# Kernel tuning notes

Measured on AMD Instinct MI355X. Metric: run time of the kernel, lower is better.

Reference implementation:

```python
import jax, jax.numpy as jnp
import numpy as np

LAMBDA_REG = 1.0  # default lambda_reg in MetaOptNetHead_Ridge_CS


def setup_inputs() -> dict:
    key = jax.random.key(0)
    k1, k2, k3 = jax.random.split(key, 3)
    B, n_query, n_support, d = 512, 75, 25, 1024
    n_way, n_shot = 5, 5
    query = jax.random.normal(k1, (B, n_query, d), dtype=jnp.float32)
    support = jax.random.normal(k2, (B, n_support, d), dtype=jnp.float32)
    support_labels = jax.random.randint(k3, (B, n_support), 0, n_way, dtype=jnp.int64)
    scale = jnp.ones((1,), dtype=jnp.float32)
    return {
        "query": query,
        "support": support,
        "support_labels": support_labels,
        "scale": scale,
        "n_way": n_way,
        "n_shot": n_shot,
    }


def reference(query, support, support_labels, scale, n_way, n_shot):
    # query:   (B, n_query, d)
    # support: (B, n_support, d), n_support == n_way * n_shot
    B, n_support, d = support.shape
    dtype = support.dtype
    # one-hot support labels: (B, n_support, n_way)
    Y = jax.nn.one_hot(support_labels, n_way, dtype=dtype)
    # K = S S^T + lambda I : (B, n_support, n_support)
    K = jnp.einsum("bnd,bmd->bnm", support, support) \
        + LAMBDA_REG * jnp.eye(n_support, dtype=dtype)
    # close_w = S^T K^{-1} Y  (computed via batched solve instead of explicit inverse)
    A = jnp.linalg.solve(K, Y)                    # (B, n_support, n_way)
    W = jnp.einsum("bnd,bnc->bdc", support, A)    # (B, d, n_way)
    logits = jnp.einsum("bqd,bdc->bqc", query, W)  # (B, n_query, n_way)
    return scale * logits
```

## Files before the change

kernel.cpp:

```cpp
#include <hip/hip_runtime.h>
#include <hip/hip_bf16.h>

#define NS 25
#define NW 5
#define D  1024
#define NQ 75
#define CHUNK 128
#define SPAD 132
#define NCHUNK (D / CHUNK)
#define WROW 1056

__global__ __launch_bounds__(256) void k_solve(const float* __restrict__ S,
                                               const int* __restrict__ labels,
                                               float* __restrict__ A_ws) {
    const int b = blockIdx.x;
    const int t = threadIdx.x;

    __shared__ float s_chunk[NS * SPAD];
    __shared__ float kpart[8 * NS * NS];
    __shared__ float M[NS * 33];
    __shared__ float prow[32];
    __shared__ float pcol[NS];

    const float* Sb = S + (size_t)b * NS * D;

    float acc[5][5];
    const int tile = t >> 3;
    const int sk   = t & 7;
    const int i0 = (tile / 5) * 5;
    const int j0 = (tile % 5) * 5;
    if (t < 200) {
#pragma unroll
        for (int a = 0; a < 5; ++a)
#pragma unroll
            for (int c = 0; c < 5; ++c) acc[a][c] = 0.f;
    }

    for (int ch = 0; ch < NCHUNK; ++ch) {
        for (int g = t; g < NS * 32; g += 256) {
            const int row = g >> 5;
            const int c4  = g & 31;
            float4 v = *reinterpret_cast<const float4*>(Sb + row * D + ch * CHUNK + c4 * 4);
            *reinterpret_cast<float4*>(&s_chunk[row * SPAD + c4 * 4]) = v;
        }
        __syncthreads();
        if (t < 200) {
#pragma unroll
            for (int ii = 0; ii < 4; ++ii) {
                const int kl = sk * 16 + ii * 4;
                float4 si[5], sj[5];
#pragma unroll
                for (int a = 0; a < 5; ++a)
                    si[a] = *reinterpret_cast<const float4*>(&s_chunk[(i0 + a) * SPAD + kl]);
#pragma unroll
                for (int a = 0; a < 5; ++a)
                    sj[a] = *reinterpret_cast<const float4*>(&s_chunk[(j0 + a) * SPAD + kl]);
#pragma unroll
                for (int a = 0; a < 5; ++a)
#pragma unroll
                    for (int c = 0; c < 5; ++c)
                        acc[a][c] += si[a].x * sj[c].x + si[a].y * sj[c].y +
                                     si[a].z * sj[c].z + si[a].w * sj[c].w;
            }
        }
        __syncthreads();
    }

    if (t < 200) {
#pragma unroll
        for (int a = 0; a < 5; ++a)
#pragma unroll
            for (int c = 0; c < 5; ++c)
                kpart[sk * NS * NS + (i0 + a) * NS + (j0 + c)] = acc[a][c];
    }
    __syncthreads();

    for (int item = t; item < NS * NS; item += 256) {
        const int i = item / NS, j = item % NS;
        float s = 0.f;
#pragma unroll
        for (int p = 0; p < 8; ++p) s += kpart[p * NS * NS + item];
        if (i == j) s += 1.0f;
        M[i * 33 + j] = s;
    }
    if (t < NS * NW) {
        const int i = t / NW, c = t % NW;
        const int lab = labels[b * NS + i];
        M[i * 33 + NS + c] = (lab == c) ? 1.f : 0.f;
    }
    __syncthreads();

    for (int p = 0; p < NS; ++p) {
        if (t < 30) prow[t] = M[p * 33 + t];
        if (t >= 32 && t < 32 + NS) pcol[t - 32] = M[(t - 32) * 33 + p];
        __syncthreads();
        const float finv = 1.0f / prow[p];
        for (int item = t; item < NS * 30; item += 256) {
            const int r = item / 30, c = item % 30;
            if (r == p) M[r * 33 + c] = prow[c] * finv;
            else        M[r * 33 + c] = M[r * 33 + c] - pcol[r] * finv * prow[c];
        }
        __syncthreads();
    }

    if (t < NS * NW) {
        A_ws[(size_t)b * NS * NW + t] = M[(t / NW) * 33 + NS + (t % NW)];
    }
}

__global__ __launch_bounds__(640) void k_logits(const float* __restrict__ Q,
                                                const float* __restrict__ S,
                                                const float* __restrict__ A_ws,
                                                const float* __restrict__ scale,
                                                float* __restrict__ out) {
    const int b = blockIdx.x;
    const int t = threadIdx.x;

    __shared__ float s_chunk[NS * SPAD];
    __shared__ float Wl[NW * WROW];
    __shared__ float A_s[NS * NW];
    __shared__ float part[NQ * NW * 8];

    const float* Sb = S + (size_t)b * NS * D;
    const float* Qb = Q + (size_t)b * NQ * D;

    if (t < NS * NW) A_s[t] = A_ws[(size_t)b * NS * NW + t];
    __syncthreads();

    for (int ch = 0; ch < NCHUNK; ++ch) {
        for (int g = t; g < NS * 32; g += 640) {
            const int row = g >> 5;
            const int c4  = g & 31;
            *reinterpret_cast<float4*>(&s_chunk[row * SPAD + c4 * 4]) =
                *reinterpret_cast<const float4*>(Sb + row * D + ch * CHUNK + c4 * 4);
        }
        __syncthreads();
        {
            const int c  = t / CHUNK;
            const int kl = t % CHUNK;
            float sum = 0.f;
#pragma unroll
            for (int j = 0; j < NS; ++j) sum += A_s[j * NW + c] * s_chunk[j * SPAD + kl];
            const int k = ch * CHUNK + kl;
            Wl[c * WROW + k + 4 * (k >> 7)] = sum;
        }
        __syncthreads();
    }

    float acc[NW] = {0.f, 0.f, 0.f, 0.f, 0.f};
    const int q  = t >> 3;
    const int ks = t & 7;
    if (q < NQ) {
        const float* qrow = Qb + q * D + ks * CHUNK;
        const int wbase = ks * CHUNK + 4 * ks;
#pragma unroll 4
        for (int i = 0; i < 32; ++i) {
            const float4 qv = *reinterpret_cast<const float4*>(qrow + i * 4);
            const int wi = wbase + i * 4;
#pragma unroll
            for (int c = 0; c < NW; ++c) {
                const float4 wv = *reinterpret_cast<const float4*>(&Wl[c * WROW + wi]);
                acc[c] += qv.x * wv.x + qv.y * wv.y + qv.z * wv.z + qv.w * wv.w;
            }
        }
#pragma unroll
        for (int c = 0; c < NW; ++c) part[(q * NW + c) * 8 + ks] = acc[c];
    }
    __syncthreads();

    if (t < NQ * NW) {
        float s = 0.f;
#pragma unroll
        for (int p = 0; p < 8; ++p) s += part[t * 8 + p];
        out[(size_t)b * NQ * NW + t] = s * scale[0];
    }
}

extern "C" void kernel_launch(void* const* d_in, const int* in_sizes, int n_in,
                              void* d_out, int out_size, void* d_ws, size_t ws_size,
                              hipStream_t stream) {
    const float* Q      = (const float*)d_in[0];
    const float* S      = (const float*)d_in[1];
    const int*   labels = (const int*)d_in[2];
    const float* scale  = (const float*)d_in[3];
    const int B = in_sizes[1] / (NS * D);

    float* A_ws = (float*)d_ws;

    k_solve<<<B, 256, 0, stream>>>(S, labels, A_ws);
    k_logits<<<B, 640, 0, stream>>>(Q, S, A_ws, scale, (float*)d_out);
}
```

Baseline: 310.9 us.

## Double-buffer S and Q loads, exploit Gram symmetry, restructure logits kernel

k_solve now prefetches S chunks into registers and double-buffered LDS with one barrier per chunk, and computes only the upper-triangular 5x5 tiles of the symmetric Gram matrix (120 threads instead of 200), mirroring at reduction time. k_logits drops to 320 threads and uses global_load_lds async DMA with double buffering for both S chunks and query rows. Each wave reduces one query row with shuffles instead of going through a partial-sum LDS buffer. This is meant to hide global memory latency and cut redundant FLOPs, but it relies on hand-placed waitcnt/barrier sequencing, which is fragile.

```diff
diff --git a/kernel.cpp b/kernel.cpp
--- a/kernel.cpp
+++ b/kernel.cpp
@@ -5,10 +5,13 @@
 #define NW 5
 #define D  1024
 #define NQ 75
-#define CHUNK 128
 #define SPAD 132
-#define NCHUNK (D / CHUNK)
-#define WROW 1056
+
+__device__ __forceinline__ void async_ld16(const float* gsrc, float* ldst) {
+    __builtin_amdgcn_global_load_lds(
+        (const __attribute__((address_space(1))) void*)gsrc,
+        (__attribute__((address_space(3))) void*)ldst, 16, 0, 0);
+}
 
 __global__ __launch_bounds__(256) void k_solve(const float* __restrict__ S,
                                                const int* __restrict__ labels,
@@ -16,45 +19,52 @@
     const int b = blockIdx.x;
     const int t = threadIdx.x;
 
-    __shared__ float s_chunk[NS * SPAD];
-    __shared__ float kpart[8 * NS * NS];
+    __shared__ float s_chunk[2][NS * SPAD];
+    __shared__ float kpart[8][NS * NS];
     __shared__ float M[NS * 33];
     __shared__ float prow[32];
     __shared__ float pcol[NS];
 
-    const float* Sb = S + (size_t)b * NS * D;
-
-    float acc[5][5];
+    const float4* Sb4 = (const float4*)(S + (size_t)b * NS * D);
+
+    float4 r0, r1, r2, r3 = make_float4(0.f, 0.f, 0.f, 0.f);
+    auto LOADC = [&](int ch) {
+        r0 = Sb4[((t      ) >> 5) * 256 + ch * 32 + ((t      ) & 31)];
+        r1 = Sb4[((t + 256) >> 5) * 256 + ch * 32 + ((t + 256) & 31)];
+        r2 = Sb4[((t + 512) >> 5) * 256 + ch * 32 + ((t + 512) & 31)];
+        if (t < 32) r3 = Sb4[((t + 768) >> 5) * 256 + ch * 32 + ((t + 768) & 31)];
+    };
+    auto WRITEC = [&](int bb) {
+        *(float4*)&s_chunk[bb][((t      ) >> 5) * SPAD + ((t      ) & 31) * 4] = r0;
+        *(float4*)&s_chunk[bb][((t + 256) >> 5) * SPAD + ((t + 256) & 31) * 4] = r1;
+        *(float4*)&s_chunk[bb][((t + 512) >> 5) * SPAD + ((t + 512) & 31) * 4] = r2;
+        if (t < 32)
+            *(float4*)&s_chunk[bb][((t + 768) >> 5) * SPAD + ((t + 768) & 31) * 4] = r3;
+    };
+
     const int tile = t >> 3;
     const int sk   = t & 7;
-    const int i0 = (tile / 5) * 5;
-    const int j0 = (tile % 5) * 5;
-    if (t < 200) {
-#pragma unroll
-        for (int a = 0; a < 5; ++a)
-#pragma unroll
-            for (int c = 0; c < 5; ++c) acc[a][c] = 0.f;
-    }
-
-    for (int ch = 0; ch < NCHUNK; ++ch) {
-        for (int g = t; g < NS * 32; g += 256) {
-            const int row = g >> 5;
-            const int c4  = g & 31;
-            float4 v = *reinterpret_cast<const float4*>(Sb + row * D + ch * CHUNK + c4 * 4);
-            *reinterpret_cast<float4*>(&s_chunk[row * SPAD + c4 * 4]) = v;
-        }
-        __syncthreads();
-        if (t < 200) {
+    const int ti = (tile < 5) ? 0 : (tile < 9) ? 1 : (tile < 12) ? 2 : (tile < 14) ? 3 : 4;
+    const int tbase = (ti == 0) ? 0 : (ti == 1) ? 5 : (ti == 2) ? 9 : (ti == 3) ? 12 : 14;
+    const int tj = ti + (tile - tbase);
+    const int i0 = ti * 5, j0 = tj * 5;
+    float acc[5][5] = {};
+
+    LOADC(0); WRITEC(0); LOADC(1);
+    asm volatile("s_waitcnt lgkmcnt(0)" ::: "memory");
+    __builtin_amdgcn_s_barrier();
+
+    for (int ch = 0; ch < 8; ++ch) {
+        if (t < 120) {
+            const float* sc_ = s_chunk[ch & 1];
 #pragma unroll
             for (int ii = 0; ii < 4; ++ii) {
-                const int kl = sk * 16 + ii * 4;
+                const int kl = sk * 4 + ii * 32;
                 float4 si[5], sj[5];
 #pragma unroll
-                for (int a = 0; a < 5; ++a)
-                    si[a] = *reinterpret_cast<const float4*>(&s_chunk[(i0 + a) * SPAD + kl]);
-#pragma unroll
-                for (int a = 0; a < 5; ++a)
-                    sj[a] = *reinterpret_cast<const float4*>(&s_chunk[(j0 + a) * SPAD + kl]);
+                for (int a = 0; a < 5; ++a) si[a] = *(const float4*)&sc_[(i0 + a) * SPAD + kl];
+#pragma unroll
+                for (int c = 0; c < 5; ++c) sj[c] = *(const float4*)&sc_[(j0 + c) * SPAD + kl];
 #pragma unroll
                 for (int a = 0; a < 5; ++a)
 #pragma unroll
@@ -63,30 +73,33 @@
                                      si[a].z * sj[c].z + si[a].w * sj[c].w;
             }
         }
-        __syncthreads();
-    }
-
-    if (t < 200) {
+        if (ch + 1 < 8) WRITEC((ch + 1) & 1);
+        if (ch + 2 < 8) LOADC(ch + 2);
+        asm volatile("s_waitcnt lgkmcnt(0)" ::: "memory");
+        __builtin_amdgcn_s_barrier();
+    }
+
+    if (t < 120) {
 #pragma unroll
         for (int a = 0; a < 5; ++a)
 #pragma unroll
             for (int c = 0; c < 5; ++c)
-                kpart[sk * NS * NS + (i0 + a) * NS + (j0 + c)] = acc[a][c];
+                kpart[sk][(i0 + a) * NS + (j0 + c)] = acc[a][c];
     }
     __syncthreads();
 
     for (int item = t; item < NS * NS; item += 256) {
         const int i = item / NS, j = item % NS;
+        const int ii = min(i, j), jj = max(i, j);
         float s = 0.f;
 #pragma unroll
-        for (int p = 0; p < 8; ++p) s += kpart[p * NS * NS + item];
+        for (int p = 0; p < 8; ++p) s += kpart[p][ii * NS + jj];
         if (i == j) s += 1.0f;
         M[i * 33 + j] = s;
     }
     if (t < NS * NW) {
         const int i = t / NW, c = t % NW;
-        const int lab = labels[b * NS + i];
-        M[i * 33 + NS + c] = (lab == c) ? 1.f : 0.f;
+        M[i * 33 + NS + c] = (labels[b * NS + i] == c) ? 1.f : 0.f;
     }
     __syncthreads();
 
@@ -96,84 +109,125 @@
         __syncthreads();
         const float finv = 1.0f / prow[p];
         for (int item = t; item < NS * 30; item += 256) {
-            const int r = item / 30, c = item % 30;
-            if (r == p) M[r * 33 + c] = prow[c] * finv;
-            else        M[r * 33 + c] = M[r * 33 + c] - pcol[r] * finv * prow[c];
+            const int rr = item / 30, cc = item % 30;
+            if (rr == p) M[rr * 33 + cc] = prow[cc] * finv;
+            else         M[rr * 33 + cc] = M[rr * 33 + cc] - pcol[rr] * finv * prow[cc];
         }
         __syncthreads();
     }
 
-    if (t < NS * NW) {
+    if (t < NS * NW)
         A_ws[(size_t)b * NS * NW + t] = M[(t / NW) * 33 + NS + (t % NW)];
-    }
-}
-
-__global__ __launch_bounds__(640) void k_logits(const float* __restrict__ Q,
+}
+
+__global__ __launch_bounds__(320) void k_logits(const float* __restrict__ Q,
                                                 const float* __restrict__ S,
                                                 const float* __restrict__ A_ws,
                                                 const float* __restrict__ scale,
                                                 float* __restrict__ out) {
     const int b = blockIdx.x;
     const int t = threadIdx.x;
-
-    __shared__ float s_chunk[NS * SPAD];
-    __shared__ float Wl[NW * WROW];
-    __shared__ float A_s[NS * NW];
-    __shared__ float part[NQ * NW * 8];
-
-    const float* Sb = S + (size_t)b * NS * D;
-    const float* Qb = Q + (size_t)b * NQ * D;
+    const int wbase = t & ~63;
+    const int l = t & 63;
+    const int w = t >> 6;
+
+    __shared__ float4 qt[2][1280];
+    __shared__ float  Wl[NW * 1024];
+    __shared__ float  A_s[128];
+    __shared__ float  outbuf[NQ * NW];
+    __shared__ float  scsh;
+
+    float* qtf = (float*)qt;
+    const float4* Sb4 = (const float4*)(S + (size_t)b * NS * D);
+    const float4* Qb4 = (const float4*)(Q + (size_t)b * NQ * D);
 
     if (t < NS * NW) A_s[t] = A_ws[(size_t)b * NS * NW + t];
-    __syncthreads();
-
-    for (int ch = 0; ch < NCHUNK; ++ch) {
-        for (int g = t; g < NS * 32; g += 640) {
-            const int row = g >> 5;
-            const int c4  = g & 31;
-            *reinterpret_cast<float4*>(&s_chunk[row * SPAD + c4 * 4]) =
-                *reinterpret_cast<const float4*>(Sb + row * D + ch * CHUNK + c4 * 4);
-        }
-        __syncthreads();
-        {
-            const int c  = t / CHUNK;
-            const int kl = t % CHUNK;
+    if (t == 0) scsh = scale[0];
+    __syncthreads();
+
+    auto dma_s = [&](int ch, int bb) {
+#pragma unroll
+        for (int it = 0; it < 3; ++it) {
+            int g = it * 320 + t;
+            int gc = (g < 800) ? g : 799;
+            const float* src = (const float*)&Sb4[(gc >> 5) * 256 + ch * 32 + (gc & 31)];
+            float* dst = qtf + bb * 3840 + (it * 320 + wbase) * 4;
+            async_ld16(src, dst);
+        }
+    };
+
+    dma_s(0, 0); dma_s(1, 1);
+    for (int ch = 0; ch < 8; ++ch) {
+        if (ch < 7) asm volatile("s_waitcnt vmcnt(3)" ::: "memory");
+        else        asm volatile("s_waitcnt vmcnt(0)" ::: "memory");
+        __builtin_amdgcn_s_barrier();
+        const float* sc_ = qtf + (ch & 1) * 3840;
+#pragma unroll
+        for (int it = 0; it < 2; ++it) {
+            const int item = it * 320 + t;
+            const int c = item >> 7, kl = item & 127;
             float sum = 0.f;
 #pragma unroll
-            for (int j = 0; j < NS; ++j) sum += A_s[j * NW + c] * s_chunk[j * SPAD + kl];
-            const int k = ch * CHUNK + kl;
-            Wl[c * WROW + k + 4 * (k >> 7)] = sum;
-        }
-        __syncthreads();
-    }
-
-    float acc[NW] = {0.f, 0.f, 0.f, 0.f, 0.f};
-    const int q  = t >> 3;
-    const int ks = t & 7;
-    if (q < NQ) {
-        const float* qrow = Qb + q * D + ks * CHUNK;
-        const int wbase = ks * CHUNK + 4 * ks;
-#pragma unroll 4
-        for (int i = 0; i < 32; ++i) {
-            const float4 qv = *reinterpret_cast<const float4*>(qrow + i * 4);
-            const int wi = wbase + i * 4;
-#pragma unroll
-            for (int c = 0; c < NW; ++c) {
-                const float4 wv = *reinterpret_cast<const float4*>(&Wl[c * WROW + wi]);
-                acc[c] += qv.x * wv.x + qv.y * wv.y + qv.z * wv.z + qv.w * wv.w;
-            }
-        }
-#pragma unroll
-        for (int c = 0; c < NW; ++c) part[(q * NW + c) * 8 + ks] = acc[c];
-    }
-    __syncthreads();
-
-    if (t < NQ * NW) {
-        float s = 0.f;
-#pragma unroll
-        for (int p = 0; p < 8; ++p) s += part[t * 8 + p];
-        out[(size_t)b * NQ * NW + t] = s * scale[0];
-    }
+            for (int j = 0; j < NS; ++j) sum += A_s[j * NW + c] * sc_[j * 128 + kl];
+            Wl[c * 1024 + ch * 128 + kl] = sum;
+        }
+        asm volatile("s_waitcnt lgkmcnt(0)" ::: "memory");
+        __builtin_amdgcn_s_barrier();
+        if (ch + 2 < 8) dma_s(ch + 2, ch & 1);
+    }
+
+    auto dma_q = [&](int tp, int bb) {
+#pragma unroll
+        for (int it = 0; it < 4; ++it) {
+            int g = it * 320 + t;
+            const float* src = (const float*)&Qb4[(tp * 5 + (g >> 8)) * 256 + (g & 255)];
+            float* dst = (float*)qt[bb] + (it * 320 + wbase) * 4;
+            async_ld16(src, dst);
+        }
+    };
+
+    dma_q(0, 0); dma_q(1, 1);
+    const float4* WL4 = (const float4*)Wl;
+    const float4* W0 = WL4, *W1 = WL4 + 256, *W2 = WL4 + 512, *W3 = WL4 + 768, *W4 = WL4 + 1024;
+
+    for (int tp = 0; tp < 15; ++tp) {
+        if (tp < 14) asm volatile("s_waitcnt vmcnt(4)" ::: "memory");
+        else         asm volatile("s_waitcnt vmcnt(0)" ::: "memory");
+        __builtin_amdgcn_s_barrier();
+        const float4* qr = qt[tp & 1] + w * 256;
+        float a0 = 0.f, a1 = 0.f, a2 = 0.f, a3 = 0.f, a4 = 0.f;
+#pragma unroll
+        for (int i = 0; i < 4; ++i) {
+            const int o = i * 64 + l;
+            const float4 qv = qr[o];
+            const float4 w0 = W0[o], w1 = W1[o], w2 = W2[o], w3 = W3[o], w4 = W4[o];
+            a0 += qv.x * w0.x + qv.y * w0.y + qv.z * w0.z + qv.w * w0.w;
+            a1 += qv.x * w1.x + qv.y * w1.y + qv.z * w1.z + qv.w * w1.w;
+            a2 += qv.x * w2.x + qv.y * w2.y + qv.z * w2.z + qv.w * w2.w;
+            a3 += qv.x * w3.x + qv.y * w3.y + qv.z * w3.z + qv.w * w3.w;
+            a4 += qv.x * w4.x + qv.y * w4.y + qv.z * w4.z + qv.w * w4.w;
+        }
+#pragma unroll
+        for (int m = 32; m >= 1; m >>= 1) {
+            a0 += __shfl_xor(a0, m);
+            a1 += __shfl_xor(a1, m);
+            a2 += __shfl_xor(a2, m);
+            a3 += __shfl_xor(a3, m);
+            a4 += __shfl_xor(a4, m);
+        }
+        if (l == 0) {
+            const int r = tp * 5 + w;
+            outbuf[r * NW + 0] = a0; outbuf[r * NW + 1] = a1; outbuf[r * NW + 2] = a2;
+            outbuf[r * NW + 3] = a3; outbuf[r * NW + 4] = a4;
+        }
+        __builtin_amdgcn_s_barrier();
+        if (tp + 2 < 15) dma_q(tp + 2, tp & 1);
+    }
+
+    __syncthreads();
+    const float scv = scsh;
+    for (int i = t; i < NQ * NW; i += 320)
+        out[(size_t)b * NQ * NW + i] = outbuf[i] * scv;
 }
 
 extern "C" void kernel_launch(void* const* d_in, const int* in_sizes, int n_in,
@@ -188,5 +242,5 @@
     float* A_ws = (float*)d_ws;
 
     k_solve<<<B, 256, 0, stream>>>(S, labels, A_ws);
-    k_logits<<<B, 640, 0, stream>>>(Q, S, A_ws, scale, (float*)d_out);
-}
+    k_logits<<<B, 320, 0, stream>>>(Q, S, A_ws, scale, (float*)d_out);
+}
```

Result: faster. 303.1 us (-2.5%).
